# Kernel optimization log

Measured on AMD Instinct MI355X. Metric: run time of the kernel, lower is better.

Reference implementation:

```python
import jax, jax.numpy as jnp
import numpy as np

N_NODES = 100000
N_EDGES = 3200000
D_FEAT = 512
HIDDEN = 16
CLASSES = 40


def gcn_conv(x, edge_index, W, b):
    """PyG GCNConv: add self-loops, sym-normalize, transform, aggregate."""
    n = x.shape[0]
    loop = jnp.arange(n, dtype=edge_index.dtype)
    src = jnp.concatenate([edge_index[0], loop])
    dst = jnp.concatenate([edge_index[1], loop])
    # degree of A + I over destination nodes
    deg = jax.ops.segment_sum(jnp.ones_like(dst, dtype=x.dtype), dst, num_segments=n)
    dinv = jnp.where(deg > 0, jax.lax.rsqrt(deg), 0.0)
    norm = dinv[src] * dinv[dst]  # [E+N]
    h = x @ W  # transform first (out_dim small)
    msg = h[src] * norm[:, None]  # gather + edge weight
    out = jax.ops.segment_sum(msg, dst, num_segments=n)  # scatter-add
    return out + b


def setup_inputs() -> dict:
    key = jax.random.key(0)
    k1, k2, k3, k4 = jax.random.split(key, 4)
    x = jax.random.normal(k1, (N_NODES, D_FEAT), dtype=jnp.float32)
    edge_index = jax.random.randint(k2, (2, N_EDGES), 0, N_NODES, dtype=jnp.int64)
    W1 = jax.random.normal(k3, (D_FEAT, HIDDEN), dtype=jnp.float32) * (1.0 / np.sqrt(D_FEAT))
    b1 = jnp.zeros((HIDDEN,), dtype=jnp.float32)
    W2 = jax.random.normal(k4, (HIDDEN, CLASSES), dtype=jnp.float32) * (1.0 / np.sqrt(HIDDEN))
    b2 = jnp.zeros((CLASSES,), dtype=jnp.float32)
    return {"x": x, "edge_index": edge_index, "W1": W1, "b1": b1, "W2": W2, "b2": b2}


def reference(x, edge_index, W1, b1, W2, b2):
    h = gcn_conv(x, edge_index, W1, b1)
    h = jax.nn.relu(h)
    # F.dropout(training=self.training): inference mode -> identity
    h = gcn_conv(h, edge_index, W2, b2)
    return jax.nn.log_softmax(h, axis=1)
```

## Files before the change

kernel.cpp:

```cpp
#include <hip/hip_runtime.h>
#include <math.h>

typedef unsigned int u32;

constexpr int NN = 100000;
constexpr int NE = 3200000;
constexpr int DF = 512;
constexpr int NH = 16;
constexpr int NC = 40;

constexpr int NB  = 512;
constexpr int BSZ = 196;
constexpr int CAP = 7168;
constexpr int SCHUNK = 16384;
constexpr int SGRID  = (NE + SCHUNK - 1) / SCHUNK;

__device__ __forceinline__ u32 pack_bf2(float lo, float hi) {
    u32 a = __float_as_uint(lo), b = __float_as_uint(hi);
    a += 0x7FFFu + ((a >> 16) & 1u);
    b += 0x7FFFu + ((b >> 16) & 1u);
    return (a >> 16) | (b & 0xFFFF0000u);
}
__device__ __forceinline__ float bf_lo(u32 u) { return __uint_as_float(u << 16); }
__device__ __forceinline__ float bf_hi(u32 u) { return __uint_as_float(u & 0xFFFF0000u); }

__global__ void k_init(int* __restrict__ gcur) {
    int i = blockIdx.x * blockDim.x + threadIdx.x;
    if (i < NB) gcur[i] = i * CAP;
}

__global__ __launch_bounds__(1024) void k_scatter_bucket(
    const int* __restrict__ src, const int* __restrict__ dst,
    int* __restrict__ gcur, u32* __restrict__ pairs) {
    __shared__ int hist[NB];
    __shared__ int gpos[NB];
    __shared__ int lcur[NB];
    const int t = threadIdx.x;
    for (int i = t; i < NB; i += 1024) { hist[i] = 0; lcur[i] = 0; }
    __syncthreads();

    const int base = blockIdx.x * SCHUNK;
    int dr[SCHUNK / 1024], sr[SCHUNK / 1024];
    #pragma unroll
    for (int k = 0; k < SCHUNK / 1024; ++k) {
        const int i = base + k * 1024 + t;
        if (i < NE) {
            dr[k] = dst[i];
            sr[k] = src[i];
            atomicAdd(&hist[(unsigned)dr[k] / BSZ], 1);
        }
    }
    __syncthreads();
    for (int i = t; i < NB; i += 1024)
        if (hist[i]) gpos[i] = atomicAdd(&gcur[i], hist[i]);
    __syncthreads();
    #pragma unroll
    for (int k = 0; k < SCHUNK / 1024; ++k) {
        const int i = base + k * 1024 + t;
        if (i < NE) {
            const unsigned d = (unsigned)dr[k];
            const unsigned b = d / BSZ;
            const unsigned dl = d - b * BSZ;
            const int off = atomicAdd(&lcur[b], 1);
            pairs[gpos[b] + off] = (unsigned)sr[k] | (dl << 17);
        }
    }
}

__global__ __launch_bounds__(1024) void k_sort_bucket(
    const u32* __restrict__ pairs, const int* __restrict__ gcur,
    int* __restrict__ esrc_s, int* __restrict__ row_start,
    int* __restrict__ degs, float* __restrict__ dinv) {
    __shared__ int hist[BSZ];
    __shared__ int scan[256];
    __shared__ int cur[BSZ];
    const int b = blockIdx.x, t = threadIdx.x;
    if (t < BSZ) hist[t] = 0;
    __syncthreads();

    const int base = b * CAP;
    const int end  = gcur[b];
    for (int p = base + t; p < end; p += 1024)
        atomicAdd(&hist[pairs[p] >> 17], 1);
    __syncthreads();

    const int h = (t < BSZ) ? hist[t] : 0;
    if (t < 256) scan[t] = (t < BSZ) ? h : 0;
    __syncthreads();
    #pragma unroll
    for (int off = 1; off < 256; off <<= 1) {
        int u = 0;
        if (t < 256 && t >= off) u = scan[t - off];
        __syncthreads();
        if (t < 256) scan[t] += u;
        __syncthreads();
    }
    if (t < BSZ) {
        const int st = scan[t] - h;
        cur[t] = st;
        const int n = b * BSZ + t;
        if (n < NN) {
            row_start[n] = base + st;
            degs[n] = h;
            dinv[n] = rsqrtf((float)(h + 1));
        }
    }
    __syncthreads();
    for (int p = base + t; p < end; p += 1024) {
        const u32 u = pairs[p];
        const int dl = u >> 17;
        const int pos = atomicAdd(&cur[dl], 1);
        esrc_s[base + pos] = (int)(u & 0x1FFFFu);
    }
}

__global__ __launch_bounds__(256) void k_gemm1(
    const float* __restrict__ x, const float* __restrict__ W1,
    const float* __restrict__ dinv, u32* __restrict__ h1b) {
    __shared__ float sX[64 * 65];
    __shared__ float sW[64 * 16];
    const int t    = threadIdx.x;
    const int lane = t & 63;
    const int og   = t >> 6;

    const int row0 = blockIdx.x * 64;
    const int lr = t >> 2, cq = t & 3;
    const bool rv = (row0 + lr) < NN;
    const float* xrow = x + (size_t)(row0 + lr) * DF + cq * 16;

    float4 pf[4];
    #pragma unroll
    for (int j = 0; j < 4; ++j)
        pf[j] = rv ? *(const float4*)&xrow[4 * j] : make_float4(0.f, 0.f, 0.f, 0.f);
    float4 wpf = *(const float4*)&W1[t * 4];

    float a0 = 0.f, a1 = 0.f, a2 = 0.f, a3 = 0.f;

    for (int kc = 0; kc < DF; kc += 64) {
        #pragma unroll
        for (int j = 0; j < 4; ++j) {
            const int kb = cq * 16 + 4 * j;
            sX[lr * 65 + kb + 0] = pf[j].x;
            sX[lr * 65 + kb + 1] = pf[j].y;
            sX[lr * 65 + kb + 2] = pf[j].z;
            sX[lr * 65 + kb + 3] = pf[j].w;
        }
        *(float4*)&sW[t * 4] = wpf;
        __syncthreads();
        if (kc + 64 < DF) {
            #pragma unroll
            for (int j = 0; j < 4; ++j)
                pf[j] = rv ? *(const float4*)&xrow[kc + 64 + 4 * j]
                           : make_float4(0.f, 0.f, 0.f, 0.f);
            wpf = *(const float4*)&W1[(kc + 64) * NH + t * 4];
        }
        #pragma unroll
        for (int k = 0; k < 64; ++k) {
            const float xv = sX[lane * 65 + k];
            const float4 wv = *(const float4*)&sW[k * NH + og * 4];
            a0 = fmaf(xv, wv.x, a0);
            a1 = fmaf(xv, wv.y, a1);
            a2 = fmaf(xv, wv.z, a2);
            a3 = fmaf(xv, wv.w, a3);
        }
        __syncthreads();
    }
    const int gr = row0 + lane;
    if (gr < NN) {
        const float s = dinv[gr];
        const u32 w0 = pack_bf2(a0 * s, a1 * s);
        const u32 w1 = pack_bf2(a2 * s, a3 * s);
        *(uint2*)&h1b[(size_t)gr * 8 + og * 2] = make_uint2(w0, w1);
    }
}

__global__ __launch_bounds__(1024) void k_agg1(
    const int* __restrict__ row_start, const int* __restrict__ degs,
    const int* __restrict__ esrc_s, const u32* __restrict__ h1b,
    const float* __restrict__ dinv, const float* __restrict__ b1,
    u32* __restrict__ A1) {
    const int node = blockIdx.x * 16 + (threadIdx.x >> 6);
    if (node >= NN) return;
    const int lane = threadIdx.x & 63;
    const int l = lane & 7;
    const int g = lane >> 3;
    const int beg = row_start[node];
    const int end = beg + degs[node];

    float a0 = 0.f, a1 = 0.f;
    int e = beg + g;
    for (; e + 8 < end; e += 16) {
        const int s0 = esrc_s[e];
        const int s1 = esrc_s[e + 8];
        const u32 u0 = h1b[(size_t)s0 * 8 + l];
        const u32 u1 = h1b[(size_t)s1 * 8 + l];
        a0 += bf_lo(u0); a1 += bf_hi(u0);
        a0 += bf_lo(u1); a1 += bf_hi(u1);
    }
    if (e < end) {
        const u32 u0 = h1b[(size_t)esrc_s[e] * 8 + l];
        a0 += bf_lo(u0); a1 += bf_hi(u0);
    }
    a0 += __shfl_xor(a0, 8);  a1 += __shfl_xor(a1, 8);
    a0 += __shfl_xor(a0, 16); a1 += __shfl_xor(a1, 16);
    a0 += __shfl_xor(a0, 32); a1 += __shfl_xor(a1, 32);

    if (g == 0) {
        const float dn = dinv[node];
        const u32 su = h1b[(size_t)node * 8 + l];
        const float p0 = (a0 + bf_lo(su)) * dn + b1[2 * l];
        const float p1 = (a1 + bf_hi(su)) * dn + b1[2 * l + 1];
        A1[(size_t)node * 8 + l] = pack_bf2(fmaxf(p0, 0.f) * dn, fmaxf(p1, 0.f) * dn);
    }
}

__global__ __launch_bounds__(1024) void k_agg2_final(
    const int* __restrict__ row_start, const int* __restrict__ degs,
    const int* __restrict__ esrc_s, const u32* __restrict__ A1,
    const float* __restrict__ dinv, const float* __restrict__ W2,
    const float* __restrict__ b2, float* __restrict__ out) {
    __shared__ float sW2[NH * NC];
    __shared__ float sb2[NC];
    const int t = threadIdx.x;
    if (t < NH * NC) sW2[t] = W2[t];
    if (t >= 1024 - NC) sb2[t - (1024 - NC)] = b2[t - (1024 - NC)];
    __syncthreads();

    const int node = blockIdx.x * 16 + (t >> 6);
    if (node >= NN) return;
    const int lane = t & 63;
    const int l = lane & 7;
    const int g = lane >> 3;
    const int beg = row_start[node];
    const int end = beg + degs[node];

    float a0 = 0.f, a1 = 0.f;
    int e = beg + g;
    for (; e + 8 < end; e += 16) {
        const int s0 = esrc_s[e];
        const int s1 = esrc_s[e + 8];
        const u32 u0 = A1[(size_t)s0 * 8 + l];
        const u32 u1 = A1[(size_t)s1 * 8 + l];
        a0 += bf_lo(u0); a1 += bf_hi(u0);
        a0 += bf_lo(u1); a1 += bf_hi(u1);
    }
    if (e < end) {
        const u32 u0 = A1[(size_t)esrc_s[e] * 8 + l];
        a0 += bf_lo(u0); a1 += bf_hi(u0);
    }
    a0 += __shfl_xor(a0, 8);  a1 += __shfl_xor(a1, 8);
    a0 += __shfl_xor(a0, 16); a1 += __shfl_xor(a1, 16);
    a0 += __shfl_xor(a0, 32); a1 += __shfl_xor(a1, 32);

    const float dn = dinv[node];
    const u32 su = A1[(size_t)node * 8 + l];
    const float ag0 = (a0 + bf_lo(su)) * dn;
    const float ag1 = (a1 + bf_hi(su)) * dn;

    float z = (lane < NC) ? sb2[lane] : -1e30f;
    #pragma unroll
    for (int k = 0; k < 8; ++k) {
        const float v0 = __shfl(ag0, k);
        const float v1 = __shfl(ag1, k);
        if (lane < NC) {
            z = fmaf(v0, sW2[(2 * k) * NC + lane], z);
            z = fmaf(v1, sW2[(2 * k + 1) * NC + lane], z);
        }
    }
    float m = z;
    #pragma unroll
    for (int off = 1; off < 64; off <<= 1) m = fmaxf(m, __shfl_xor(m, off));
    float sum = (lane < NC) ? __expf(z - m) : 0.f;
    #pragma unroll
    for (int off = 1; off < 64; off <<= 1) sum += __shfl_xor(sum, off);
    const float lse = m + __logf(sum);
    if (lane < NC) out[(size_t)node * NC + lane] = z - lse;
}

extern "C" void kernel_launch(void* const* d_in, const int* in_sizes, int n_in,
                              void* d_out, int out_size, void* d_ws, size_t ws_size,
                              hipStream_t stream) {
    const float* x  = (const float*)d_in[0];
    const int*   ei = (const int*)d_in[1];
    const float* W1 = (const float*)d_in[2];
    const float* b1 = (const float*)d_in[3];
    const float* W2 = (const float*)d_in[4];
    const float* b2 = (const float*)d_in[5];
    float* out = (float*)d_out;

    int* gcur      = (int*)d_ws;
    u32* pairs     = (u32*)(gcur + NB);
    int* esrc_s    = (int*)(pairs + (size_t)NB * CAP);
    int* row_start = esrc_s + (size_t)NB * CAP;
    int* degs      = row_start + NN;
    float* dinv    = (float*)(degs + NN);
    u32* h1b       = (u32*)(dinv + NN);
    u32* A1        = h1b + (size_t)NN * 8;

    const int* esrc = ei;
    const int* edst = ei + NE;

    k_init          <<<(NB + 255) / 256, 256, 0, stream>>>(gcur);
    k_scatter_bucket<<<SGRID, 1024, 0, stream>>>(esrc, edst, gcur, pairs);
    k_sort_bucket   <<<NB, 1024, 0, stream>>>(pairs, gcur, esrc_s, row_start, degs, dinv);
    k_gemm1         <<<(NN + 63) / 64, 256, 0, stream>>>(x, W1, dinv, h1b);
    k_agg1          <<<(NN + 15) / 16, 1024, 0, stream>>>(row_start, degs, esrc_s, h1b, dinv, b1, A1);
    k_agg2_final    <<<(NN + 15) / 16, 1024, 0, stream>>>(row_start, degs, esrc_s, A1, dinv, W2, b2, out);
}
```

Before: 213.2 us.

## Retile first-layer GEMM to 128 rows per block with swizzled float4 LDS

```diff
diff --git a/kernel.cpp b/kernel.cpp
--- a/kernel.cpp
+++ b/kernel.cpp
@@ -114,63 +114,80 @@
     }
 }
 
-__global__ __launch_bounds__(256) void k_gemm1(
+__global__ __launch_bounds__(256, 4) void k_gemm1(
     const float* __restrict__ x, const float* __restrict__ W1,
     const float* __restrict__ dinv, u32* __restrict__ h1b) {
-    __shared__ float sX[64 * 65];
-    __shared__ float sW[64 * 16];
+    __shared__ __align__(16) float sX[128 * 64];
+    __shared__ __align__(16) float sW[64 * NH];
     const int t    = threadIdx.x;
     const int lane = t & 63;
-    const int og   = t >> 6;
-
-    const int row0 = blockIdx.x * 64;
-    const int lr = t >> 2, cq = t & 3;
-    const bool rv = (row0 + lr) < NN;
-    const float* xrow = x + (size_t)(row0 + lr) * DF + cq * 16;
-
-    float4 pf[4];
-    #pragma unroll
-    for (int j = 0; j < 4; ++j)
-        pf[j] = rv ? *(const float4*)&xrow[4 * j] : make_float4(0.f, 0.f, 0.f, 0.f);
+    const int og   = __builtin_amdgcn_readfirstlane(t >> 6);
+
+    const int row0 = blockIdx.x * 128;
+    const int lr = t >> 1, hf = t & 1;
+    const bool lv = (row0 + lr) < NN;
+    const float* xrow = x + (size_t)(row0 + lr) * DF + hf * 32;
+
+    float4 pf[8];
+    #pragma unroll
+    for (int j = 0; j < 8; ++j)
+        pf[j] = lv ? *(const float4*)&xrow[4 * j] : make_float4(0.f, 0.f, 0.f, 0.f);
     float4 wpf = *(const float4*)&W1[t * 4];
 
+    const int r0 = lane, r1 = lane + 64;
+    const int sw0 = r0 & 7;
     float a0 = 0.f, a1 = 0.f, a2 = 0.f, a3 = 0.f;
+    float c0 = 0.f, c1 = 0.f, c2 = 0.f, c3 = 0.f;
 
     for (int kc = 0; kc < DF; kc += 64) {
         #pragma unroll
-        for (int j = 0; j < 4; ++j) {
-            const int kb = cq * 16 + 4 * j;
-            sX[lr * 65 + kb + 0] = pf[j].x;
-            sX[lr * 65 + kb + 1] = pf[j].y;
-            sX[lr * 65 + kb + 2] = pf[j].z;
-            sX[lr * 65 + kb + 3] = pf[j].w;
+        for (int j = 0; j < 8; ++j) {
+            const int g = hf * 8 + j;
+            const int slot = g ^ (lr & 7);
+            *(float4*)&sX[lr * 64 + slot * 4] = pf[j];
         }
         *(float4*)&sW[t * 4] = wpf;
         __syncthreads();
         if (kc + 64 < DF) {
             #pragma unroll
-            for (int j = 0; j < 4; ++j)
-                pf[j] = rv ? *(const float4*)&xrow[kc + 64 + 4 * j]
+            for (int j = 0; j < 8; ++j)
+                pf[j] = lv ? *(const float4*)&xrow[kc + 64 + 4 * j]
                            : make_float4(0.f, 0.f, 0.f, 0.f);
             wpf = *(const float4*)&W1[(kc + 64) * NH + t * 4];
         }
         #pragma unroll
-        for (int k = 0; k < 64; ++k) {
-            const float xv = sX[lane * 65 + k];
-            const float4 wv = *(const float4*)&sW[k * NH + og * 4];
-            a0 = fmaf(xv, wv.x, a0);
-            a1 = fmaf(xv, wv.y, a1);
-            a2 = fmaf(xv, wv.z, a2);
-            a3 = fmaf(xv, wv.w, a3);
+        for (int g = 0; g < 16; ++g) {
+            const float4 x0 = *(const float4*)&sX[r0 * 64 + (g ^ sw0) * 4];
+            const float4 x1 = *(const float4*)&sX[r1 * 64 + (g ^ sw0) * 4];
+            const float xa0[4] = {x0.x, x0.y, x0.z, x0.w};
+            const float xa1[4] = {x1.x, x1.y, x1.z, x1.w};
+            #pragma unroll
+            for (int j = 0; j < 4; ++j) {
+                const int k = g * 4 + j;
+                const float4 wv = *(const float4*)&sW[k * NH + og * 4];
+                a0 = fmaf(xa0[j], wv.x, a0);
+                a1 = fmaf(xa0[j], wv.y, a1);
+                a2 = fmaf(xa0[j], wv.z, a2);
+                a3 = fmaf(xa0[j], wv.w, a3);
+                c0 = fmaf(xa1[j], wv.x, c0);
+                c1 = fmaf(xa1[j], wv.y, c1);
+                c2 = fmaf(xa1[j], wv.z, c2);
+                c3 = fmaf(xa1[j], wv.w, c3);
+            }
         }
         __syncthreads();
     }
-    const int gr = row0 + lane;
-    if (gr < NN) {
-        const float s = dinv[gr];
-        const u32 w0 = pack_bf2(a0 * s, a1 * s);
-        const u32 w1 = pack_bf2(a2 * s, a3 * s);
-        *(uint2*)&h1b[(size_t)gr * 8 + og * 2] = make_uint2(w0, w1);
+    const int gr0 = row0 + r0;
+    const int gr1 = row0 + r1;
+    if (gr0 < NN) {
+        const float s = dinv[gr0];
+        *(uint2*)&h1b[(size_t)gr0 * 8 + og * 2] =
+            make_uint2(pack_bf2(a0 * s, a1 * s), pack_bf2(a2 * s, a3 * s));
+    }
+    if (gr1 < NN) {
+        const float s = dinv[gr1];
+        *(uint2*)&h1b[(size_t)gr1 * 8 + og * 2] =
+            make_uint2(pack_bf2(c0 * s, c1 * s), pack_bf2(c2 * s, c3 * s));
     }
 }
 
@@ -303,7 +320,7 @@
     k_init          <<<(NB + 255) / 256, 256, 0, stream>>>(gcur);
     k_scatter_bucket<<<SGRID, 1024, 0, stream>>>(esrc, edst, gcur, pairs);
     k_sort_bucket   <<<NB, 1024, 0, stream>>>(pairs, gcur, esrc_s, row_start, degs, dinv);
-    k_gemm1         <<<(NN + 63) / 64, 256, 0, stream>>>(x, W1, dinv, h1b);
+    k_gemm1         <<<(NN + 127) / 128, 256, 0, stream>>>(x, W1, dinv, h1b);
     k_agg1          <<<(NN + 15) / 16, 1024, 0, stream>>>(row_start, degs, esrc_s, h1b, dinv, b1, A1);
     k_agg2_final    <<<(NN + 15) / 16, 1024, 0, stream>>>(row_start, degs, esrc_s, A1, dinv, W2, b2, out);
 }
```

After: 382.3 us. 79.3% more time.
